# Performance work log

Hardware: AMD Instinct MI355X
Metric: run time of the kernel (lower is better)

## Reference

```python
import jax, jax.numpy as jnp
import numpy as np

GENOMES, BATCH, SEQ, EMBED = 8, 2, 2048, 1024
HEADS, KV_HEADS = 16, 4
HEAD_DIM = EMBED // HEADS  # 64
RATIO = HEADS // KV_HEADS  # 4
CONSTANT = 10000.0


def _rope_tables(seq_len, head_dim, constant):
    theta = constant ** (-2.0 * jnp.arange(0, head_dim, 2, dtype=jnp.float32) / head_dim)
    angles = jnp.arange(seq_len, dtype=jnp.float32)[:, None] * theta[None, :]  # [S, hd/2]
    return jnp.cos(angles), jnp.sin(angles)


def _apply_rope(x, cos, sin):
    # x: [g,b,s,h,hd]; treat last dim as hd/2 complex pairs, rotate by angle per (s, pair)
    g, b, s, h, hd = x.shape
    xr = x.reshape(g, b, s, h, hd // 2, 2)
    x0, x1 = xr[..., 0], xr[..., 1]
    c = cos[None, None, :, None, :]
    sn = sin[None, None, :, None, :]
    o0 = x0 * c - x1 * sn
    o1 = x0 * sn + x1 * c
    return jnp.stack([o0, o1], axis=-1).reshape(g, b, s, h, hd)


def setup_inputs() -> dict:
    key = jax.random.key(0)
    ks = jax.random.split(key, 5)
    scale = 0.02
    return {
        "tensor": jax.random.normal(ks[0], (GENOMES, BATCH, SEQ, EMBED), dtype=jnp.float32),
        "Wq": jax.random.normal(ks[1], (GENOMES, EMBED, HEADS * HEAD_DIM), dtype=jnp.float32) * scale,
        "Wk": jax.random.normal(ks[2], (GENOMES, EMBED, KV_HEADS * HEAD_DIM), dtype=jnp.float32) * scale,
        "Wv": jax.random.normal(ks[3], (GENOMES, EMBED, KV_HEADS * HEAD_DIM), dtype=jnp.float32) * scale,
        "Wo": jax.random.normal(ks[4], (GENOMES, EMBED, EMBED), dtype=jnp.float32) * scale,
    }


def reference(tensor, Wq, Wk, Wv, Wo):
    g, b, s, _ = tensor.shape
    cos, sin = _rope_tables(SEQ, HEAD_DIM, CONSTANT)
    # per-genome linear projections
    q = jnp.einsum('gbsi,gio->gbso', tensor, Wq).reshape(g, b, s, HEADS, HEAD_DIM)
    k = jnp.einsum('gbsi,gio->gbso', tensor, Wk).reshape(g, b, s, KV_HEADS, HEAD_DIM)
    v = jnp.einsum('gbsi,gio->gbso', tensor, Wv).reshape(g, b, s, KV_HEADS, HEAD_DIM)
    q = _apply_rope(q, cos, sin)
    k = _apply_rope(k, cos, sin)
    # repeat_kv: [g,b,s,kvh,hd] -> [g,b,s,kvh*ratio,hd]
    k = jnp.broadcast_to(k[:, :, :, :, None, :], (g, b, s, KV_HEADS, RATIO, HEAD_DIM)).reshape(g, b, s, HEADS, HEAD_DIM)
    v = jnp.broadcast_to(v[:, :, :, :, None, :], (g, b, s, KV_HEADS, RATIO, HEAD_DIM)).reshape(g, b, s, HEADS, HEAD_DIM)
    # NOTE: faithful to the original (non-standard) einsums: contraction over seq in QK^T,
    # energy is [g,b,h,head_dim,head_dim]
    energy = jnp.einsum('gbshq,gbshk->gbhqk', q, k)
    scores = jax.nn.softmax(energy / jnp.sqrt(jnp.float32(HEAD_DIM)), axis=-1)
    # attention = value scaled by total score mass per (g,b,h)
    attention = jnp.einsum('gbhqk,gbshv->gbshv', scores, v)
    attention = attention.reshape(g, b, s, EMBED)
    return jnp.einsum('gbsi,gio->gbso', attention, Wo)
```

## Files before the change

### kernel.cpp

```cpp
#include <hip/hip_runtime.h>
#include <stdint.h>

#define GENOMES 8
#define BATCH 2
#define SEQ 2048
#define EMBED 1024
#define KVD 256
#define M_PER_G (BATCH*SEQ)

typedef float f32x4 __attribute__((ext_vector_type(4)));
typedef __bf16 bf16x8 __attribute__((ext_vector_type(8)));
typedef short s16x8 __attribute__((ext_vector_type(8)));
typedef short s16x4 __attribute__((ext_vector_type(4)));

static __device__ __forceinline__ unsigned short f2bf(float f) {
  unsigned int u = __builtin_bit_cast(unsigned int, f);
  u += 0x7FFFu + ((u >> 16) & 1u);
  return (unsigned short)(u >> 16);
}

__global__ __launch_bounds__(256) void wvt_kernel(const float* __restrict__ Wv,
                                                  unsigned short* __restrict__ WvT) {
  int g = blockIdx.y;
  int it = blockIdx.x >> 2;
  int ot = blockIdx.x & 3;
  int i0 = it * 64, o0 = ot * 64;
  const float* W = Wv + (size_t)g * EMBED * KVD;
  unsigned short* T = WvT + (size_t)g * KVD * EMBED;
  __shared__ unsigned short tl[64][65];
  int t = threadIdx.x;
  int rr = t >> 4;
  int cc = (t & 15) * 4;
#pragma unroll
  for (int p = 0; p < 4; ++p) {
    int r = rr + p * 16;
    float4 v = *(const float4*)(W + (size_t)(i0 + r) * KVD + o0 + cc);
    tl[r][cc + 0] = f2bf(v.x);
    tl[r][cc + 1] = f2bf(v.y);
    tl[r][cc + 2] = f2bf(v.z);
    tl[r][cc + 3] = f2bf(v.w);
  }
  __syncthreads();
#pragma unroll
  for (int p = 0; p < 4; ++p) {
    int o = rr + p * 16;
    s16x4 v;
    v[0] = (short)tl[cc + 0][o];
    v[1] = (short)tl[cc + 1][o];
    v[2] = (short)tl[cc + 2][o];
    v[3] = (short)tl[cc + 3][o];
    *(s16x4*)(T + (size_t)(o0 + o) * EMBED + i0 + cc) = v;
  }
}

__global__ __launch_bounds__(256) void rt_kernel(const float* __restrict__ Wo,
                                                 unsigned short* __restrict__ RT) {
  int g = blockIdx.y;
  int ot = blockIdx.x >> 2;
  int kh = blockIdx.x & 3;
  int o0 = ot * 64;
  const float* W = Wo + (size_t)g * EMBED * EMBED;
  unsigned short* T = RT + (size_t)g * EMBED * KVD;
  __shared__ float tl[64][65];
  int t = threadIdx.x;
  int rr = t >> 4;
  int cc = (t & 15) * 4;
#pragma unroll
  for (int p = 0; p < 4; ++p) {
    int d = rr + p * 16;
    float a0 = 0.f, a1 = 0.f, a2 = 0.f, a3 = 0.f;
#pragma unroll
    for (int r = 0; r < 4; ++r) {
      float4 v = *(const float4*)(W + (size_t)(kh * 256 + r * 64 + d) * EMBED + o0 + cc);
      a0 += v.x; a1 += v.y; a2 += v.z; a3 += v.w;
    }
    tl[d][cc + 0] = a0; tl[d][cc + 1] = a1; tl[d][cc + 2] = a2; tl[d][cc + 3] = a3;
  }
  __syncthreads();
#pragma unroll
  for (int p = 0; p < 4; ++p) {
    int o = rr + p * 16;
    s16x4 v;
    v[0] = (short)f2bf(64.f * tl[cc + 0][o]);
    v[1] = (short)f2bf(64.f * tl[cc + 1][o]);
    v[2] = (short)f2bf(64.f * tl[cc + 2][o]);
    v[3] = (short)f2bf(64.f * tl[cc + 3][o]);
    *(s16x4*)(T + (size_t)(o0 + o) * KVD + kh * 64 + cc) = v;
  }
}

template <bool A_F32, bool OUT_BF16, int M, int N, int K>
__global__ __launch_bounds__(256) void gemm_bt(const void* __restrict__ Aall,
                                               const unsigned short* __restrict__ Btall,
                                               void* __restrict__ Call) {
  constexpr int BK = 32;
  int g = blockIdx.y;
  constexpr int NTILES = N / 128;
  int bm = blockIdx.x / NTILES;
  int bn = blockIdx.x % NTILES;
  int m0 = bm * 128, n0 = bn * 128;
  const unsigned short* Bt = Btall + (size_t)g * N * K;
  const float* Af = (const float*)Aall + (size_t)g * M * K;
  const unsigned short* Ab = (const unsigned short*)Aall + (size_t)g * M * K;

  __shared__ unsigned short As[128][BK];
  __shared__ unsigned short Bs[128][BK];

  int t = threadIdx.x;
  int lane = t & 63, wave = t >> 6;
  int wm = (wave >> 1) * 64, wn = (wave & 1) * 64;
  int lm = lane & 15, quad = lane >> 4;
  int kq = quad * 8;

  f32x4 acc[4][4] = {};

  for (int k0 = 0; k0 < K; k0 += BK) {
    if constexpr (A_F32) {
      int row = t >> 3, col = (t & 7) * 4;
#pragma unroll
      for (int p = 0; p < 4; ++p) {
        int r = row + p * 32;
        float4 v = *(const float4*)(Af + (size_t)(m0 + r) * K + k0 + col);
        s16x4 b;
        b[0] = (short)f2bf(v.x); b[1] = (short)f2bf(v.y);
        b[2] = (short)f2bf(v.z); b[3] = (short)f2bf(v.w);
        *(s16x4*)&As[r][col] = b;
      }
    } else {
      int row = t >> 2, col = (t & 3) * 8;
#pragma unroll
      for (int p = 0; p < 2; ++p) {
        int r = row + p * 64;
        s16x8 v = *(const s16x8*)(Ab + (size_t)(m0 + r) * K + k0 + col);
        *(s16x8*)&As[r][col] = v;
      }
    }
    {
      int row = t >> 2, col = (t & 3) * 8;
#pragma unroll
      for (int p = 0; p < 2; ++p) {
        int r = row + p * 64;
        s16x8 v = *(const s16x8*)(Bt + (size_t)(n0 + r) * K + k0 + col);
        *(s16x8*)&Bs[r][col] = v;
      }
    }
    __syncthreads();

    bf16x8 af[4], bfr[4];
#pragma unroll
    for (int i = 0; i < 4; ++i) {
      af[i]  = __builtin_bit_cast(bf16x8, *(const s16x8*)&As[wm + i * 16 + lm][kq]);
      bfr[i] = __builtin_bit_cast(bf16x8, *(const s16x8*)&Bs[wn + i * 16 + lm][kq]);
    }
#pragma unroll
    for (int i = 0; i < 4; ++i)
#pragma unroll
      for (int j = 0; j < 4; ++j)
        acc[i][j] = __builtin_amdgcn_mfma_f32_16x16x32_bf16(af[i], bfr[j], acc[i][j], 0, 0, 0);
    __syncthreads();
  }

  if constexpr (OUT_BF16) {
    unsigned short* C = (unsigned short*)Call + (size_t)g * M * N;
#pragma unroll
    for (int i = 0; i < 4; ++i)
#pragma unroll
      for (int j = 0; j < 4; ++j)
#pragma unroll
        for (int r = 0; r < 4; ++r) {
          int mm = m0 + wm + i * 16 + quad * 4 + r;
          int nn = n0 + wn + j * 16 + lm;
          C[(size_t)mm * N + nn] = f2bf(acc[i][j][r]);
        }
  } else {
    float* C = (float*)Call + (size_t)g * M * N;
#pragma unroll
    for (int i = 0; i < 4; ++i)
#pragma unroll
      for (int j = 0; j < 4; ++j)
#pragma unroll
        for (int r = 0; r < 4; ++r) {
          int mm = m0 + wm + i * 16 + quad * 4 + r;
          int nn = n0 + wn + j * 16 + lm;
          C[(size_t)mm * N + nn] = acc[i][j][r];
        }
  }
}

extern "C" void kernel_launch(void* const* d_in, const int* in_sizes, int n_in,
                              void* d_out, int out_size, void* d_ws, size_t ws_size,
                              hipStream_t stream) {
  const float* tensor = (const float*)d_in[0];
  const float* Wv = (const float*)d_in[3];
  const float* Wo = (const float*)d_in[4];
  float* out = (float*)d_out;

  unsigned short* WvT = (unsigned short*)d_ws;
  unsigned short* RT  = WvT + (size_t)GENOMES * KVD * EMBED;
  unsigned short* V   = RT  + (size_t)GENOMES * EMBED * KVD;

  wvt_kernel<<<dim3(64, GENOMES), 256, 0, stream>>>(Wv, WvT);
  rt_kernel<<<dim3(64, GENOMES), 256, 0, stream>>>(Wo, RT);

  gemm_bt<true, true, M_PER_G, KVD, EMBED>
      <<<dim3((M_PER_G / 128) * (KVD / 128), GENOMES), 256, 0, stream>>>(tensor, WvT, V);

  gemm_bt<false, false, M_PER_G, EMBED, KVD>
      <<<dim3((M_PER_G / 128) * (EMBED / 128), GENOMES), 256, 0, stream>>>(V, RT, out);
}
```

Measured before the change: 331.3 us.

## Prefetch next K-tile into registers, pad LDS rows, shrink first GEMM tile

The GEMM main loop now issues the global loads for the next K-tile into registers before running the MFMAs on the current tile, so load latency can overlap with compute. Shared-memory rows are padded from 32 to 48 elements to cut bank conflicts on fragment reads. The first GEMM (N=256) uses a 64-row M tile, which doubles its block count for better CU occupancy. The cost is more registers for the prefetch buffers and somewhat more LDS per block.

```diff
diff --git a/kernel.cpp b/kernel.cpp
--- a/kernel.cpp
+++ b/kernel.cpp
@@ -89,81 +89,105 @@
   }
 }
 
-template <bool A_F32, bool OUT_BF16, int M, int N, int K>
+template <bool A_F32, bool OUT_BF16, int BM, int M, int N, int K>
 __global__ __launch_bounds__(256) void gemm_bt(const void* __restrict__ Aall,
                                                const unsigned short* __restrict__ Btall,
                                                void* __restrict__ Call) {
   constexpr int BK = 32;
+  constexpr int LDA = BK + 16;
+  constexpr int MI = BM / 32;
+  constexpr int NT = N / 128;
+  constexpr int NKT = K / BK;
+
   int g = blockIdx.y;
-  constexpr int NTILES = N / 128;
-  int bm = blockIdx.x / NTILES;
-  int bn = blockIdx.x % NTILES;
-  int m0 = bm * 128, n0 = bn * 128;
+  int bm = blockIdx.x / NT;
+  int bn = blockIdx.x % NT;
+  int m0 = bm * BM, n0 = bn * 128;
   const unsigned short* Bt = Btall + (size_t)g * N * K;
   const float* Af = (const float*)Aall + (size_t)g * M * K;
   const unsigned short* Ab = (const unsigned short*)Aall + (size_t)g * M * K;
 
-  __shared__ unsigned short As[128][BK];
-  __shared__ unsigned short Bs[128][BK];
+  __shared__ unsigned short As[BM][LDA];
+  __shared__ unsigned short Bs[128][LDA];
 
   int t = threadIdx.x;
   int lane = t & 63, wave = t >> 6;
-  int wm = (wave >> 1) * 64, wn = (wave & 1) * 64;
+  int wm = (wave >> 1) * (BM / 2), wn = (wave & 1) * 64;
   int lm = lane & 15, quad = lane >> 4;
   int kq = quad * 8;
 
-  f32x4 acc[4][4] = {};
-
-  for (int k0 = 0; k0 < K; k0 += BK) {
+  f32x4 acc[MI][4] = {};
+
+  float4 paf[MI];
+  s16x8 pab[BM / 64];
+  s16x8 pb[2];
+
+  auto loadTile = [&](int k0) {
     if constexpr (A_F32) {
       int row = t >> 3, col = (t & 7) * 4;
 #pragma unroll
-      for (int p = 0; p < 4; ++p) {
-        int r = row + p * 32;
-        float4 v = *(const float4*)(Af + (size_t)(m0 + r) * K + k0 + col);
+      for (int p = 0; p < MI; ++p)
+        paf[p] = *(const float4*)(Af + (size_t)(m0 + row + p * 32) * K + k0 + col);
+    } else {
+      int row = t >> 2, col = (t & 3) * 8;
+#pragma unroll
+      for (int p = 0; p < BM / 64; ++p)
+        pab[p] = *(const s16x8*)(Ab + (size_t)(m0 + row + p * 64) * K + k0 + col);
+    }
+    int row = t >> 2, col = (t & 3) * 8;
+#pragma unroll
+    for (int p = 0; p < 2; ++p)
+      pb[p] = *(const s16x8*)(Bt + (size_t)(n0 + row + p * 64) * K + k0 + col);
+  };
+
+  auto storeLDS = [&]() {
+    if constexpr (A_F32) {
+      int row = t >> 3, col = (t & 7) * 4;
+#pragma unroll
+      for (int p = 0; p < MI; ++p) {
         s16x4 b;
-        b[0] = (short)f2bf(v.x); b[1] = (short)f2bf(v.y);
-        b[2] = (short)f2bf(v.z); b[3] = (short)f2bf(v.w);
-        *(s16x4*)&As[r][col] = b;
+        b[0] = (short)f2bf(paf[p].x); b[1] = (short)f2bf(paf[p].y);
+        b[2] = (short)f2bf(paf[p].z); b[3] = (short)f2bf(paf[p].w);
+        *(s16x4*)&As[row + p * 32][col] = b;
       }
     } else {
       int row = t >> 2, col = (t & 3) * 8;
 #pragma unroll
-      for (int p = 0; p < 2; ++p) {
-        int r = row + p * 64;
-        s16x8 v = *(const s16x8*)(Ab + (size_t)(m0 + r) * K + k0 + col);
-        *(s16x8*)&As[r][col] = v;
-      }
+      for (int p = 0; p < BM / 64; ++p)
+        *(s16x8*)&As[row + p * 64][col] = pab[p];
     }
-    {
-      int row = t >> 2, col = (t & 3) * 8;
-#pragma unroll
-      for (int p = 0; p < 2; ++p) {
-        int r = row + p * 64;
-        s16x8 v = *(const s16x8*)(Bt + (size_t)(n0 + r) * K + k0 + col);
-        *(s16x8*)&Bs[r][col] = v;
-      }
-    }
+    int row = t >> 2, col = (t & 3) * 8;
+#pragma unroll
+    for (int p = 0; p < 2; ++p)
+      *(s16x8*)&Bs[row + p * 64][col] = pb[p];
+  };
+
+  loadTile(0);
+  for (int kt = 0; kt < NKT; ++kt) {
     __syncthreads();
-
-    bf16x8 af[4], bfr[4];
-#pragma unroll
-    for (int i = 0; i < 4; ++i) {
-      af[i]  = __builtin_bit_cast(bf16x8, *(const s16x8*)&As[wm + i * 16 + lm][kq]);
-      bfr[i] = __builtin_bit_cast(bf16x8, *(const s16x8*)&Bs[wn + i * 16 + lm][kq]);
-    }
-#pragma unroll
-    for (int i = 0; i < 4; ++i)
+    storeLDS();
+    __syncthreads();
+    int kn = (kt + 1 < NKT ? kt + 1 : kt) * BK;
+    loadTile(kn);
+
+    bf16x8 af[MI], bfr[4];
+#pragma unroll
+    for (int i = 0; i < MI; ++i)
+      af[i] = __builtin_bit_cast(bf16x8, *(const s16x8*)&As[wm + i * 16 + lm][kq]);
+#pragma unroll
+    for (int j = 0; j < 4; ++j)
+      bfr[j] = __builtin_bit_cast(bf16x8, *(const s16x8*)&Bs[wn + j * 16 + lm][kq]);
+#pragma unroll
+    for (int i = 0; i < MI; ++i)
 #pragma unroll
       for (int j = 0; j < 4; ++j)
         acc[i][j] = __builtin_amdgcn_mfma_f32_16x16x32_bf16(af[i], bfr[j], acc[i][j], 0, 0, 0);
-    __syncthreads();
   }
 
   if constexpr (OUT_BF16) {
     unsigned short* C = (unsigned short*)Call + (size_t)g * M * N;
 #pragma unroll
-    for (int i = 0; i < 4; ++i)
+    for (int i = 0; i < MI; ++i)
 #pragma unroll
       for (int j = 0; j < 4; ++j)
 #pragma unroll
@@ -175,7 +199,7 @@
   } else {
     float* C = (float*)Call + (size_t)g * M * N;
 #pragma unroll
-    for (int i = 0; i < 4; ++i)
+    for (int i = 0; i < MI; ++i)
 #pragma unroll
       for (int j = 0; j < 4; ++j)
 #pragma unroll
@@ -202,9 +226,9 @@
   wvt_kernel<<<dim3(64, GENOMES), 256, 0, stream>>>(Wv, WvT);
   rt_kernel<<<dim3(64, GENOMES), 256, 0, stream>>>(Wo, RT);
 
-  gemm_bt<true, true, M_PER_G, KVD, EMBED>
-      <<<dim3((M_PER_G / 128) * (KVD / 128), GENOMES), 256, 0, stream>>>(tensor, WvT, V);
-
-  gemm_bt<false, false, M_PER_G, EMBED, KVD>
+  gemm_bt<true, true, 64, M_PER_G, KVD, EMBED>
+      <<<dim3((M_PER_G / 64) * (KVD / 128), GENOMES), 256, 0, stream>>>(tensor, WvT, V);
+
+  gemm_bt<false, false, 128, M_PER_G, EMBED, KVD>
       <<<dim3((M_PER_G / 128) * (EMBED / 128), GENOMES), 256, 0, stream>>>(V, RT, out);
 }
```

After: 340.3 us. +2.7%, slower.

## Replace LDS-tiled GEMM with direct-to-register loads and software double buffering

Applied to the files above, without the earlier changes.

Both GEMMs drop shared memory staging. Each wave loads its MFMA fragments straight from global memory into registers, with a two-stage prefetch so the next K-slice's loads overlap the current MFMAs. Block tiles change to 64x256 with waves split along N, and the fp32 output uses nontemporal stores. The aim is to remove LDS traffic and barriers. The cost is that A rows are loaded redundantly by each of the four waves, and the per-lane global loads are only 16-32 bytes, so they may coalesce poorly.

```diff
diff --git a/kernel.cpp b/kernel.cpp
--- a/kernel.cpp
+++ b/kernel.cpp
@@ -89,100 +89,113 @@
   }
 }
 
-template <bool A_F32, bool OUT_BF16, int M, int N, int K>
-__global__ __launch_bounds__(256) void gemm_bt(const void* __restrict__ Aall,
-                                               const unsigned short* __restrict__ Btall,
-                                               void* __restrict__ Call) {
+template <bool A_F32, bool OUT_BF16, int N, int K>
+__global__ __launch_bounds__(256) void gemm_direct(const void* __restrict__ Aall,
+                                                   const unsigned short* __restrict__ Btall,
+                                                   void* __restrict__ Call) {
   constexpr int BK = 32;
+  constexpr int NKT = K / BK;
+  constexpr int NG = N / 256;
+
   int g = blockIdx.y;
-  constexpr int NTILES = N / 128;
-  int bm = blockIdx.x / NTILES;
-  int bn = blockIdx.x % NTILES;
-  int m0 = bm * 128, n0 = bn * 128;
-  const unsigned short* Bt = Btall + (size_t)g * N * K;
-  const float* Af = (const float*)Aall + (size_t)g * M * K;
-  const unsigned short* Ab = (const unsigned short*)Aall + (size_t)g * M * K;
-
-  __shared__ unsigned short As[128][BK];
-  __shared__ unsigned short Bs[128][BK];
+  int bm = blockIdx.x / NG;
+  int bn = blockIdx.x % NG;
+  int m0 = bm * 64;
 
   int t = threadIdx.x;
   int lane = t & 63, wave = t >> 6;
-  int wm = (wave >> 1) * 64, wn = (wave & 1) * 64;
+  int n0 = bn * 256 + wave * 64;
   int lm = lane & 15, quad = lane >> 4;
   int kq = quad * 8;
 
+  const float* Af = (const float*)Aall + (size_t)g * M_PER_G * K + (size_t)(m0 + lm) * K + kq;
+  const unsigned short* Ab = (const unsigned short*)Aall + (size_t)g * M_PER_G * K + (size_t)(m0 + lm) * K + kq;
+  const unsigned short* Bt = Btall + (size_t)g * N * K + (size_t)(n0 + lm) * K + kq;
+
   f32x4 acc[4][4] = {};
 
-  for (int k0 = 0; k0 < K; k0 += BK) {
+  float4 a0f[4][2], a1f[4][2];
+  s16x8 a0b[4], a1b[4];
+  s16x8 b0[4], b1[4];
+
+  auto loadA = [&](int k0, float4 af[4][2], s16x8 ab[4]) {
     if constexpr (A_F32) {
-      int row = t >> 3, col = (t & 7) * 4;
-#pragma unroll
-      for (int p = 0; p < 4; ++p) {
-        int r = row + p * 32;
-        float4 v = *(const float4*)(Af + (size_t)(m0 + r) * K + k0 + col);
-        s16x4 b;
-        b[0] = (short)f2bf(v.x); b[1] = (short)f2bf(v.y);
-        b[2] = (short)f2bf(v.z); b[3] = (short)f2bf(v.w);
-        *(s16x4*)&As[r][col] = b;
+#pragma unroll
+      for (int i = 0; i < 4; ++i) {
+        const float* p = Af + (size_t)(i * 16) * K + k0;
+        af[i][0] = *(const float4*)p;
+        af[i][1] = *(const float4*)(p + 4);
       }
     } else {
-      int row = t >> 2, col = (t & 3) * 8;
-#pragma unroll
-      for (int p = 0; p < 2; ++p) {
-        int r = row + p * 64;
-        s16x8 v = *(const s16x8*)(Ab + (size_t)(m0 + r) * K + k0 + col);
-        *(s16x8*)&As[r][col] = v;
+#pragma unroll
+      for (int i = 0; i < 4; ++i)
+        ab[i] = *(const s16x8*)(Ab + (size_t)(i * 16) * K + k0);
+    }
+  };
+  auto loadB = [&](int k0, s16x8 b[4]) {
+#pragma unroll
+    for (int j = 0; j < 4; ++j)
+      b[j] = *(const s16x8*)(Bt + (size_t)(j * 16) * K + k0);
+  };
+  auto step = [&](float4 af[4][2], s16x8 ab[4], s16x8 b[4]) {
+    bf16x8 abf[4], bbf[4];
+#pragma unroll
+    for (int i = 0; i < 4; ++i) {
+      if constexpr (A_F32) {
+        bf16x8 c;
+        c[0] = (__bf16)af[i][0].x; c[1] = (__bf16)af[i][0].y;
+        c[2] = (__bf16)af[i][0].z; c[3] = (__bf16)af[i][0].w;
+        c[4] = (__bf16)af[i][1].x; c[5] = (__bf16)af[i][1].y;
+        c[6] = (__bf16)af[i][1].z; c[7] = (__bf16)af[i][1].w;
+        abf[i] = c;
+      } else {
+        abf[i] = __builtin_bit_cast(bf16x8, ab[i]);
       }
+      bbf[i] = __builtin_bit_cast(bf16x8, b[i]);
     }
-    {
-      int row = t >> 2, col = (t & 3) * 8;
-#pragma unroll
-      for (int p = 0; p < 2; ++p) {
-        int r = row + p * 64;
-        s16x8 v = *(const s16x8*)(Bt + (size_t)(n0 + r) * K + k0 + col);
-        *(s16x8*)&Bs[r][col] = v;
-      }
-    }
-    __syncthreads();
-
-    bf16x8 af[4], bfr[4];
-#pragma unroll
-    for (int i = 0; i < 4; ++i) {
-      af[i]  = __builtin_bit_cast(bf16x8, *(const s16x8*)&As[wm + i * 16 + lm][kq]);
-      bfr[i] = __builtin_bit_cast(bf16x8, *(const s16x8*)&Bs[wn + i * 16 + lm][kq]);
-    }
 #pragma unroll
     for (int i = 0; i < 4; ++i)
 #pragma unroll
       for (int j = 0; j < 4; ++j)
-        acc[i][j] = __builtin_amdgcn_mfma_f32_16x16x32_bf16(af[i], bfr[j], acc[i][j], 0, 0, 0);
-    __syncthreads();
+        acc[i][j] = __builtin_amdgcn_mfma_f32_16x16x32_bf16(abf[i], bbf[j], acc[i][j], 0, 0, 0);
+  };
+
+  loadA(0, a0f, a0b);
+  loadB(0, b0);
+  for (int kt = 0; kt < NKT; kt += 2) {
+    int k1 = (kt + 1 < NKT ? kt + 1 : NKT - 1) * BK;
+    loadA(k1, a1f, a1b);
+    loadB(k1, b1);
+    step(a0f, a0b, b0);
+    int k2 = (kt + 2 < NKT ? kt + 2 : NKT - 1) * BK;
+    loadA(k2, a0f, a0b);
+    loadB(k2, b0);
+    step(a1f, a1b, b1);
   }
 
   if constexpr (OUT_BF16) {
-    unsigned short* C = (unsigned short*)Call + (size_t)g * M * N;
+    unsigned short* C = (unsigned short*)Call + (size_t)g * M_PER_G * N;
 #pragma unroll
     for (int i = 0; i < 4; ++i)
 #pragma unroll
       for (int j = 0; j < 4; ++j)
 #pragma unroll
         for (int r = 0; r < 4; ++r) {
-          int mm = m0 + wm + i * 16 + quad * 4 + r;
-          int nn = n0 + wn + j * 16 + lm;
+          int mm = m0 + i * 16 + quad * 4 + r;
+          int nn = n0 + j * 16 + lm;
           C[(size_t)mm * N + nn] = f2bf(acc[i][j][r]);
         }
   } else {
-    float* C = (float*)Call + (size_t)g * M * N;
+    float* C = (float*)Call + (size_t)g * M_PER_G * N;
 #pragma unroll
     for (int i = 0; i < 4; ++i)
 #pragma unroll
       for (int j = 0; j < 4; ++j)
 #pragma unroll
         for (int r = 0; r < 4; ++r) {
-          int mm = m0 + wm + i * 16 + quad * 4 + r;
-          int nn = n0 + wn + j * 16 + lm;
-          C[(size_t)mm * N + nn] = acc[i][j][r];
+          int mm = m0 + i * 16 + quad * 4 + r;
+          int nn = n0 + j * 16 + lm;
+          __builtin_nontemporal_store(acc[i][j][r], C + (size_t)mm * N + nn);
         }
   }
 }
@@ -202,9 +215,9 @@
   wvt_kernel<<<dim3(64, GENOMES), 256, 0, stream>>>(Wv, WvT);
   rt_kernel<<<dim3(64, GENOMES), 256, 0, stream>>>(Wo, RT);
 
-  gemm_bt<true, true, M_PER_G, KVD, EMBED>
-      <<<dim3((M_PER_G / 128) * (KVD / 128), GENOMES), 256, 0, stream>>>(tensor, WvT, V);
-
-  gemm_bt<false, false, M_PER_G, EMBED, KVD>
-      <<<dim3((M_PER_G / 128) * (EMBED / 128), GENOMES), 256, 0, stream>>>(V, RT, out);
-}
+  gemm_direct<true, true, KVD, EMBED>
+      <<<dim3(M_PER_G / 64, GENOMES), 256, 0, stream>>>(tensor, WvT, V);
+
+  gemm_direct<false, false, EMBED, KVD>
+      <<<dim3((M_PER_G / 64) * (EMBED / 256), GENOMES), 256, 0, stream>>>(V, RT, out);
+}
```

Measured after the change: 459.1 us. +38.6%, slower.
